# Performance work log

Hardware: AMD Instinct MI355X
Metric: run time of the kernel (lower is better)

The kernel has to match this reference:

```python
import jax, jax.numpy as jnp
import numpy as np

B, N, D_IN, D_OUT, H = 8, 1024, 768, 768, 12
D_HEAD = D_OUT // H  # 64; per-head softmax scale is sqrt(D_HEAD)


def setup_inputs() -> dict:
    key = jax.random.key(0)
    kx, kq, kk, kv, kwo, kbo = jax.random.split(key, 6)
    s_in = 1.0 / np.sqrt(D_IN)
    s_out = 1.0 / np.sqrt(D_OUT)
    return {
        "x": jax.random.normal(kx, (B, N, D_IN), dtype=jnp.float32),
        # stacked per-head Linear weights, torch layout [out, in] -> [H, d_head, D_IN]
        "Wq": jax.random.uniform(kq, (H, D_HEAD, D_IN), jnp.float32, -s_in, s_in),
        "Wk": jax.random.uniform(kk, (H, D_HEAD, D_IN), jnp.float32, -s_in, s_in),
        "Wv": jax.random.uniform(kv, (H, D_HEAD, D_IN), jnp.float32, -s_in, s_in),
        "Wo": jax.random.uniform(kwo, (D_OUT, D_OUT), jnp.float32, -s_out, s_out),
        "bo": jax.random.uniform(kbo, (D_OUT,), jnp.float32, -s_out, s_out),
    }


def reference(x, Wq, Wk, Wv, Wo, bo):
    # Per-head projections, batched over heads: [B, H, N, d_head]
    q = jnp.einsum('bnd,hed->bhne', x, Wq)
    k = jnp.einsum('bnd,hed->bhne', x, Wk)
    v = jnp.einsum('bnd,hed->bhne', x, Wv)
    scale = 1.0 / np.sqrt(D_HEAD)
    scores = jnp.einsum('bhie,bhje->bhij', q, k) * scale  # [B, H, N, N]
    att = jax.nn.softmax(scores, axis=-1)
    out = jnp.einsum('bhij,bhje->bhie', att, v)  # [B, H, N, d_head]
    # concat heads along last dim: [B, N, H*d_head]
    out = out.transpose(0, 2, 1, 3).reshape(B, N, D_OUT)
    return out @ Wo.T + bo
```

## Files before the change

### kernel.cpp

```cpp
#include <hip/hip_runtime.h>
#include <hip/hip_bf16.h>


typedef unsigned short u16;
typedef __attribute__((ext_vector_type(8))) short bf8;
typedef __attribute__((ext_vector_type(4))) short bf4;
typedef __attribute__((ext_vector_type(4))) float f4;
typedef __attribute__((ext_vector_type(4))) unsigned short us4;

#define NB 8
#define NSEQ 1024
#define DMODEL 768
#define NHEAD 12
#define DHEAD 64

#define XELEMS   (NB * NSEQ * DMODEL)
#define WELEMS   (DMODEL * DMODEL)

__device__ __forceinline__ float b2f(u16 u) {
  union { unsigned int i; float f; } c; c.i = ((unsigned int)u) << 16; return c.f;
}
__device__ __forceinline__ u16 f2b(float f) {
  union { float f; unsigned int i; } c; c.f = f;
  unsigned int r = c.i + 0x7fffu + ((c.i >> 16) & 1u);
  return (u16)(r >> 16);
}
__device__ __forceinline__ void gl_lds16(const u16* g, u16* l) {
  __builtin_amdgcn_global_load_lds(
      (const __attribute__((address_space(1))) unsigned int*)g,
      (__attribute__((address_space(3))) unsigned int*)l, 16, 0, 0);
}

struct CvtArgs {
  const float* src[5];
  u16* dst[5];
};
#define G0 (XELEMS / 4)
#define GW (WELEMS / 4)
#define GTOT (G0 + 4 * GW)

__global__ __launch_bounds__(256) void cvt_kernel(CvtArgs a) {
  size_t g = (size_t)blockIdx.x * 256 + threadIdx.x;
  if (g >= GTOT) return;
  int t; size_t off;
  if (g < G0) { t = 0; off = g; }
  else { size_t r = g - G0; t = 1 + (int)(r / GW); off = r % GW; }
  f4 v = *(const f4*)(a.src[t] + off * 4);
  us4 o;
  o[0] = f2b(v[0]); o[1] = f2b(v[1]); o[2] = f2b(v[2]); o[3] = f2b(v[3]);
  *(us4*)(a.dst[t] + off * 4) = o;
}

__global__ __launch_bounds__(256, 4) void qkv_gemm(
    const u16* __restrict__ x, const u16* __restrict__ Wq,
    const u16* __restrict__ Wk, const u16* __restrict__ Wv,
    u16* __restrict__ q, u16* __restrict__ k, u16* __restrict__ vt)
{
  __shared__ __align__(16) u16 lA[128 * 64];
  __shared__ __align__(16) u16 lB[128 * 64];

  const int tid  = threadIdx.x;
  const int lane = tid & 63;
  const int w    = tid >> 6;
  const int wm   = w >> 1, wn = w & 1;
  const int col  = lane & 15;
  const int quad = lane >> 4;
  const int bm = blockIdx.x;
  const int bn = blockIdx.y;

  const int m0 = bm * 128;
  const int proj = bn / 6;
  const u16* Wsel = (proj == 0) ? Wq : (proj == 1 ? Wk : Wv);
  const int nrem0 = (bn % 6) * 128;

  const int krow = lane >> 3;
  const int gsrc = (lane & 7) ^ krow;
  const u16* gA0 = x    + (size_t)(m0    + w * 32 + krow) * DMODEL + gsrc * 8;
  const u16* gB0 = Wsel + (size_t)(nrem0 + w * 32 + krow) * DMODEL + gsrc * 8;

  f4 acc[4][4];
#pragma unroll
  for (int i = 0; i < 4; i++)
#pragma unroll
    for (int j = 0; j < 4; j++) acc[i][j] = (f4)0.0f;

  for (int kk = 0; kk < DMODEL; kk += 64) {
    __syncthreads();
#pragma unroll
    for (int i = 0; i < 4; i++) {
      gl_lds16(gA0 + (size_t)(i * 8) * DMODEL + kk, lA + (w * 32 + i * 8) * 64);
      gl_lds16(gB0 + (size_t)(i * 8) * DMODEL + kk, lB + (w * 32 + i * 8) * 64);
    }
    __syncthreads();

#pragma unroll
    for (int kt = 0; kt < 2; kt++) {
      bf8 af[4], bfr[4];
#pragma unroll
      for (int mt = 0; mt < 4; mt++) {
        const int row = wm * 64 + mt * 16 + col;
        af[mt] = *(const bf8*)&lA[row * 64 + (((kt * 4 + quad) ^ (row & 7)) << 3)];
      }
#pragma unroll
      for (int nt = 0; nt < 4; nt++) {
        const int row = wn * 64 + nt * 16 + col;
        bfr[nt] = *(const bf8*)&lB[row * 64 + (((kt * 4 + quad) ^ (row & 7)) << 3)];
      }
#pragma unroll
      for (int mt = 0; mt < 4; mt++)
#pragma unroll
        for (int nt = 0; nt < 4; nt++)
          acc[mt][nt] = __builtin_amdgcn_mfma_f32_16x16x32_bf16(af[mt], bfr[nt], acc[mt][nt], 0, 0, 0);
    }
  }

  const int mw0 = m0 + wm * 64, nw0 = nrem0 + wn * 64;
  if (proj == 2) {
#pragma unroll
    for (int mt = 0; mt < 4; mt++) {
#pragma unroll
      for (int nt = 0; nt < 4; nt++) {
        const int nc = nw0 + nt * 16 + col;
        const int h = nc >> 6, e = nc & 63;
        const int t0 = mw0 + mt * 16 + quad * 4;
        const int b = t0 >> 10, tok0 = t0 & 1023;
        us4 pk;
#pragma unroll
        for (int r = 0; r < 4; r++) pk[r] = f2b(acc[mt][nt][r]);
        *(us4*)(vt + ((size_t)(b * NHEAD + h) * DHEAD + e) * NSEQ + tok0) = pk;
      }
    }
  } else {
    u16* dst = (proj == 0) ? q : k;
#pragma unroll
    for (int mt = 0; mt < 4; mt++) {
#pragma unroll
      for (int nt = 0; nt < 4; nt++) {
        const int nc = nw0 + nt * 16 + col;
        const int h = nc >> 6, e = nc & 63;
#pragma unroll
        for (int r = 0; r < 4; r++) {
          const int t = mw0 + mt * 16 + quad * 4 + r;
          const int b = t >> 10, tok = t & 1023;
          dst[((size_t)(b * NHEAD + h) * NSEQ + tok) * DHEAD + e] = f2b(acc[mt][nt][r]);
        }
      }
    }
  }
}

__global__ __launch_bounds__(256, 4) void attn_kernel(
    const u16* __restrict__ q, const u16* __restrict__ k,
    const u16* __restrict__ vt, u16* __restrict__ attn)
{
  __shared__ __align__(16) u16 ldsK[64 * 64];
  __shared__ __align__(16) u16 ldsV[64 * 64];
  __shared__ __align__(16) u16 ldsP[4][16][72];

  const int tid  = threadIdx.x;
  const int lane = tid & 63;
  const int w    = tid >> 6;
  const int col  = lane & 15;
  const int quad = lane >> 4;

  const int idx = blockIdx.x;
  const int bh = idx % 96, qc = idx / 96;
  const int b = bh / 12, h = bh % 12;

  const size_t head = ((size_t)b * NHEAD + h) * NSEQ * DHEAD;
  const int q0 = qc * 128 + w * 32;

  const int srow8 = lane >> 3;
  const int sg    = (lane & 7) ^ srow8;

  bf8 onesf;
#pragma unroll
  for (int j = 0; j < 8; j++) onesf[j] = (short)0x3F80;

  bf8 qf[2][2];
#pragma unroll
  for (int mt = 0; mt < 2; mt++)
#pragma unroll
    for (int kt = 0; kt < 2; kt++) {
      const int row = q0 + mt * 16 + col;
      bf8 t = *(const bf8*)(q + head + (size_t)row * DHEAD + kt * 32 + quad * 8);
#pragma unroll
      for (int j = 0; j < 8; j++) t[j] = (short)f2b(b2f((u16)t[j]) * 0.125f);
      qf[mt][kt] = t;
    }

  f4 lacc[2];
  f4 o[2][4];
#pragma unroll
  for (int mt = 0; mt < 2; mt++) {
    lacc[mt] = (f4)0.0f;
#pragma unroll
    for (int et = 0; et < 4; et++) o[mt][et] = (f4)0.0f;
  }

  for (int t = 0; t < NSEQ / 64; t++) {
    const int kbase = t * 64;

    __syncthreads();
#pragma unroll
    for (int i = 0; i < 2; i++) {
      const int li = w * 2 + i;
      gl_lds16(k  + head + (size_t)(kbase + li * 8 + srow8) * DHEAD + sg * 8,
               &ldsK[li * 512]);
      gl_lds16(vt + head + (size_t)(li * 8 + srow8) * NSEQ + kbase + sg * 8,
               &ldsV[li * 512]);
    }
    __syncthreads();

    f4 s[2][4];
#pragma unroll
    for (int mt = 0; mt < 2; mt++)
#pragma unroll
      for (int nt = 0; nt < 4; nt++) s[mt][nt] = (f4)0.0f;
#pragma unroll
    for (int kt = 0; kt < 2; kt++) {
      bf8 kf[4];
#pragma unroll
      for (int nt = 0; nt < 4; nt++) {
        const int row = nt * 16 + col;
        kf[nt] = *(const bf8*)&ldsK[row * 64 + (((kt * 4 + quad) ^ (col & 7)) << 3)];
      }
#pragma unroll
      for (int mt = 0; mt < 2; mt++)
#pragma unroll
        for (int nt = 0; nt < 4; nt++)
          s[mt][nt] = __builtin_amdgcn_mfma_f32_16x16x32_bf16(qf[mt][kt], kf[nt], s[mt][nt], 0, 0, 0);
    }

#pragma unroll
    for (int mt = 0; mt < 2; mt++) {
#pragma unroll
      for (int nt = 0; nt < 4; nt++)
#pragma unroll
        for (int r = 0; r < 4; r++)
          ldsP[w][quad * 4 + r][nt * 16 + col] = f2b(__expf(s[mt][nt][r]));
#pragma unroll
      for (int kt2 = 0; kt2 < 2; kt2++) {
        bf8 pf, vf[4];
        {
          const u16* pp = &ldsP[w][col][kt2 * 32 + quad * 8];
          bf4 lo = *(const bf4*)pp;
          bf4 hi = *(const bf4*)(pp + 4);
          pf = bf8{lo[0], lo[1], lo[2], lo[3], hi[0], hi[1], hi[2], hi[3]};
        }
        lacc[mt] = __builtin_amdgcn_mfma_f32_16x16x32_bf16(pf, onesf, lacc[mt], 0, 0, 0);
#pragma unroll
        for (int et = 0; et < 4; et++) {
          const int row = et * 16 + col;
          vf[et] = *(const bf8*)&ldsV[row * 64 + (((kt2 * 4 + quad) ^ (col & 7)) << 3)];
        }
#pragma unroll
        for (int et = 0; et < 4; et++)
          o[mt][et] = __builtin_amdgcn_mfma_f32_16x16x32_bf16(pf, vf[et], o[mt][et], 0, 0, 0);
      }
    }
  }

#pragma unroll
  for (int mt = 0; mt < 2; mt++)
#pragma unroll
    for (int r = 0; r < 4; r++) {
      const float inv = 1.0f / lacc[mt][r];
      const int token = q0 + mt * 16 + quad * 4 + r;
#pragma unroll
      for (int et = 0; et < 4; et++)
        attn[(size_t)(b * NSEQ + token) * DMODEL + h * DHEAD + et * 16 + col] =
            f2b(o[mt][et][r] * inv);
    }
}

__global__ __launch_bounds__(256, 4) void out_gemm(
    const u16* __restrict__ attn, const u16* __restrict__ Wo,
    const float* __restrict__ bo, float* __restrict__ out)
{
  __shared__ __align__(16) u16 lA[128 * 64];
  __shared__ __align__(16) u16 lB[128 * 64];

  const int tid  = threadIdx.x;
  const int lane = tid & 63;
  const int w    = tid >> 6;
  const int wm   = w >> 1, wn = w & 1;
  const int col  = lane & 15;
  const int quad = lane >> 4;
  const int bm = blockIdx.x;
  const int bn = blockIdx.y;

  const int m0 = bm * 128;
  const int n0 = bn * 128;

  const int krow = lane >> 3;
  const int gsrc = (lane & 7) ^ krow;
  const u16* gA0 = attn + (size_t)(m0 + w * 32 + krow) * DMODEL + gsrc * 8;
  const u16* gB0 = Wo   + (size_t)(n0 + w * 32 + krow) * DMODEL + gsrc * 8;

  f4 acc[4][4];
#pragma unroll
  for (int i = 0; i < 4; i++)
#pragma unroll
    for (int j = 0; j < 4; j++) acc[i][j] = (f4)0.0f;

  for (int kk = 0; kk < DMODEL; kk += 64) {
    __syncthreads();
#pragma unroll
    for (int i = 0; i < 4; i++) {
      gl_lds16(gA0 + (size_t)(i * 8) * DMODEL + kk, lA + (w * 32 + i * 8) * 64);
      gl_lds16(gB0 + (size_t)(i * 8) * DMODEL + kk, lB + (w * 32 + i * 8) * 64);
    }
    __syncthreads();

#pragma unroll
    for (int kt = 0; kt < 2; kt++) {
      bf8 af[4], bfr[4];
#pragma unroll
      for (int mt = 0; mt < 4; mt++) {
        const int row = wm * 64 + mt * 16 + col;
        af[mt] = *(const bf8*)&lA[row * 64 + (((kt * 4 + quad) ^ (row & 7)) << 3)];
      }
#pragma unroll
      for (int nt = 0; nt < 4; nt++) {
        const int row = wn * 64 + nt * 16 + col;
        bfr[nt] = *(const bf8*)&lB[row * 64 + (((kt * 4 + quad) ^ (row & 7)) << 3)];
      }
#pragma unroll
      for (int mt = 0; mt < 4; mt++)
#pragma unroll
        for (int nt = 0; nt < 4; nt++)
          acc[mt][nt] = __builtin_amdgcn_mfma_f32_16x16x32_bf16(af[mt], bfr[nt], acc[mt][nt], 0, 0, 0);
    }
  }

  const int mw0 = m0 + wm * 64, nw0 = n0 + wn * 64;
#pragma unroll
  for (int mt = 0; mt < 4; mt++)
#pragma unroll
    for (int nt = 0; nt < 4; nt++) {
      const int n = nw0 + nt * 16 + col;
      const float bias = bo[n];
#pragma unroll
      for (int r = 0; r < 4; r++) {
        const int row = mw0 + mt * 16 + quad * 4 + r;
        out[(size_t)row * DMODEL + n] = acc[mt][nt][r] + bias;
      }
    }
}

extern "C" void kernel_launch(void* const* d_in, const int* in_sizes, int n_in,
                              void* d_out, int out_size, void* d_ws, size_t ws_size,
                              hipStream_t stream) {
  const float* x  = (const float*)d_in[0];
  const float* Wq = (const float*)d_in[1];
  const float* Wk = (const float*)d_in[2];
  const float* Wv = (const float*)d_in[3];
  const float* Wo = (const float*)d_in[4];
  const float* bo = (const float*)d_in[5];
  float* out = (float*)d_out;

  u16* xb   = (u16*)d_ws;
  u16* wqb  = xb  + XELEMS;
  u16* wkb  = wqb + WELEMS;
  u16* wvb  = wkb + WELEMS;
  u16* wob  = wvb + WELEMS;
  u16* q    = wob + WELEMS;
  u16* k    = q   + XELEMS;
  u16* vt   = k   + XELEMS;
  u16* attn = vt  + XELEMS;

  CvtArgs ca;
  ca.src[0] = x;  ca.src[1] = Wq;  ca.src[2] = Wk;  ca.src[3] = Wv;  ca.src[4] = Wo;
  ca.dst[0] = xb; ca.dst[1] = wqb; ca.dst[2] = wkb; ca.dst[3] = wvb; ca.dst[4] = wob;

  cvt_kernel<<<dim3((GTOT + 255) / 256), 256, 0, stream>>>(ca);
  qkv_gemm<<<dim3(64, 18), 256, 0, stream>>>(xb, wqb, wkb, wvb, q, k, vt);
  attn_kernel<<<dim3(768), 256, 0, stream>>>(q, k, vt, attn);
  out_gemm<<<dim3(64, 6), 256, 0, stream>>>(attn, wob, bo, out);
}
```

Measured before the change: 197.9 us.

## Double-buffer LDS tiles in QKV, attention and output kernels with prefetch

The QKV and output GEMMs now keep two LDS buffers with a K-step of 32 instead of 64, and use a new XOR swizzle for the narrower rows. They issue the global-to-LDS load for the next K slice before computing on the current one, which leaves one barrier per iteration instead of two. The attention kernel likewise double-buffers its K and V tiles to prefetch the next key block during compute. Its occupancy hint drops from 4 to 3 blocks to make room for the larger shared-memory footprint. This is meant to hide global load latency behind MFMA work, at the cost of more LDS use, twice as many GEMM iterations and barriers, and lower attention occupancy.

```diff
diff --git a/kernel.cpp b/kernel.cpp
--- a/kernel.cpp
+++ b/kernel.cpp
@@ -56,8 +56,8 @@
     const u16* __restrict__ Wk, const u16* __restrict__ Wv,
     u16* __restrict__ q, u16* __restrict__ k, u16* __restrict__ vt)
 {
-  __shared__ __align__(16) u16 lA[128 * 64];
-  __shared__ __align__(16) u16 lB[128 * 64];
+  __shared__ __align__(16) u16 lA[2][128 * 32];
+  __shared__ __align__(16) u16 lB[2][128 * 32];
 
   const int tid  = threadIdx.x;
   const int lane = tid & 63;
@@ -73,10 +73,10 @@
   const u16* Wsel = (proj == 0) ? Wq : (proj == 1 ? Wk : Wv);
   const int nrem0 = (bn % 6) * 128;
 
-  const int krow = lane >> 3;
-  const int gsrc = (lane & 7) ^ krow;
-  const u16* gA0 = x    + (size_t)(m0    + w * 32 + krow) * DMODEL + gsrc * 8;
-  const u16* gB0 = Wsel + (size_t)(nrem0 + w * 32 + krow) * DMODEL + gsrc * 8;
+  const int srow = lane >> 2;
+  const int sg   = (lane & 3) ^ ((srow >> 1) & 3);
+  const u16* gA0 = x    + (size_t)(m0    + w * 32 + srow) * DMODEL + sg * 8;
+  const u16* gB0 = Wsel + (size_t)(nrem0 + w * 32 + srow) * DMODEL + sg * 8;
 
   f4 acc[4][4];
 #pragma unroll
@@ -84,34 +84,38 @@
 #pragma unroll
     for (int j = 0; j < 4; j++) acc[i][j] = (f4)0.0f;
 
-  for (int kk = 0; kk < DMODEL; kk += 64) {
+  gl_lds16(gA0, &lA[0][(w * 32) * 32]);
+  gl_lds16(gA0 + (size_t)16 * DMODEL, &lA[0][(w * 32 + 16) * 32]);
+  gl_lds16(gB0, &lB[0][(w * 32) * 32]);
+  gl_lds16(gB0 + (size_t)16 * DMODEL, &lB[0][(w * 32 + 16) * 32]);
+
+  for (int it = 0; it < 24; it++) {
+    const int cur = it & 1;
     __syncthreads();
-#pragma unroll
-    for (int i = 0; i < 4; i++) {
-      gl_lds16(gA0 + (size_t)(i * 8) * DMODEL + kk, lA + (w * 32 + i * 8) * 64);
-      gl_lds16(gB0 + (size_t)(i * 8) * DMODEL + kk, lB + (w * 32 + i * 8) * 64);
-    }
-    __syncthreads();
-
-#pragma unroll
-    for (int kt = 0; kt < 2; kt++) {
-      bf8 af[4], bfr[4];
-#pragma unroll
-      for (int mt = 0; mt < 4; mt++) {
-        const int row = wm * 64 + mt * 16 + col;
-        af[mt] = *(const bf8*)&lA[row * 64 + (((kt * 4 + quad) ^ (row & 7)) << 3)];
-      }
-#pragma unroll
-      for (int nt = 0; nt < 4; nt++) {
-        const int row = wn * 64 + nt * 16 + col;
-        bfr[nt] = *(const bf8*)&lB[row * 64 + (((kt * 4 + quad) ^ (row & 7)) << 3)];
-      }
-#pragma unroll
-      for (int mt = 0; mt < 4; mt++)
-#pragma unroll
-        for (int nt = 0; nt < 4; nt++)
-          acc[mt][nt] = __builtin_amdgcn_mfma_f32_16x16x32_bf16(af[mt], bfr[nt], acc[mt][nt], 0, 0, 0);
-    }
+    if (it < 23) {
+      const int kk = (it + 1) * 32;
+      gl_lds16(gA0 + kk, &lA[cur ^ 1][(w * 32) * 32]);
+      gl_lds16(gA0 + (size_t)16 * DMODEL + kk, &lA[cur ^ 1][(w * 32 + 16) * 32]);
+      gl_lds16(gB0 + kk, &lB[cur ^ 1][(w * 32) * 32]);
+      gl_lds16(gB0 + (size_t)16 * DMODEL + kk, &lB[cur ^ 1][(w * 32 + 16) * 32]);
+    }
+
+    bf8 af[4], bfr[4];
+#pragma unroll
+    for (int mt = 0; mt < 4; mt++) {
+      const int row = wm * 64 + mt * 16 + col;
+      af[mt] = *(const bf8*)&lA[cur][row * 32 + ((quad ^ ((row >> 1) & 3)) << 3)];
+    }
+#pragma unroll
+    for (int nt = 0; nt < 4; nt++) {
+      const int row = wn * 64 + nt * 16 + col;
+      bfr[nt] = *(const bf8*)&lB[cur][row * 32 + ((quad ^ ((row >> 1) & 3)) << 3)];
+    }
+#pragma unroll
+    for (int mt = 0; mt < 4; mt++)
+#pragma unroll
+      for (int nt = 0; nt < 4; nt++)
+        acc[mt][nt] = __builtin_amdgcn_mfma_f32_16x16x32_bf16(af[mt], bfr[nt], acc[mt][nt], 0, 0, 0);
   }
 
   const int mw0 = m0 + wm * 64, nw0 = nrem0 + wn * 64;
@@ -149,12 +153,12 @@
   }
 }
 
-__global__ __launch_bounds__(256, 4) void attn_kernel(
+__global__ __launch_bounds__(256, 3) void attn_kernel(
     const u16* __restrict__ q, const u16* __restrict__ k,
     const u16* __restrict__ vt, u16* __restrict__ attn)
 {
-  __shared__ __align__(16) u16 ldsK[64 * 64];
-  __shared__ __align__(16) u16 ldsV[64 * 64];
+  __shared__ __align__(16) u16 ldsK[2][64 * 64];
+  __shared__ __align__(16) u16 ldsV[2][64 * 64];
   __shared__ __align__(16) u16 ldsP[4][16][72];
 
   const int tid  = threadIdx.x;
@@ -198,19 +202,27 @@
     for (int et = 0; et < 4; et++) o[mt][et] = (f4)0.0f;
   }
 
+#pragma unroll
+  for (int i = 0; i < 2; i++) {
+    const int li = w * 2 + i;
+    gl_lds16(k  + head + (size_t)(li * 8 + srow8) * DHEAD + sg * 8, &ldsK[0][li * 512]);
+    gl_lds16(vt + head + (size_t)(li * 8 + srow8) * NSEQ + sg * 8,  &ldsV[0][li * 512]);
+  }
+
   for (int t = 0; t < NSEQ / 64; t++) {
-    const int kbase = t * 64;
-
+    const int cur = t & 1;
     __syncthreads();
-#pragma unroll
-    for (int i = 0; i < 2; i++) {
-      const int li = w * 2 + i;
-      gl_lds16(k  + head + (size_t)(kbase + li * 8 + srow8) * DHEAD + sg * 8,
-               &ldsK[li * 512]);
-      gl_lds16(vt + head + (size_t)(li * 8 + srow8) * NSEQ + kbase + sg * 8,
-               &ldsV[li * 512]);
-    }
-    __syncthreads();
+    if (t < NSEQ / 64 - 1) {
+      const int kb2 = (t + 1) * 64;
+#pragma unroll
+      for (int i = 0; i < 2; i++) {
+        const int li = w * 2 + i;
+        gl_lds16(k  + head + (size_t)(kb2 + li * 8 + srow8) * DHEAD + sg * 8,
+                 &ldsK[cur ^ 1][li * 512]);
+        gl_lds16(vt + head + (size_t)(li * 8 + srow8) * NSEQ + kb2 + sg * 8,
+                 &ldsV[cur ^ 1][li * 512]);
+      }
+    }
 
     f4 s[2][4];
 #pragma unroll
@@ -223,7 +235,7 @@
 #pragma unroll
       for (int nt = 0; nt < 4; nt++) {
         const int row = nt * 16 + col;
-        kf[nt] = *(const bf8*)&ldsK[row * 64 + (((kt * 4 + quad) ^ (col & 7)) << 3)];
+        kf[nt] = *(const bf8*)&ldsK[cur][row * 64 + (((kt * 4 + quad) ^ (col & 7)) << 3)];
       }
 #pragma unroll
       for (int mt = 0; mt < 2; mt++)
@@ -252,7 +264,7 @@
 #pragma unroll
         for (int et = 0; et < 4; et++) {
           const int row = et * 16 + col;
-          vf[et] = *(const bf8*)&ldsV[row * 64 + (((kt2 * 4 + quad) ^ (col & 7)) << 3)];
+          vf[et] = *(const bf8*)&ldsV[cur][row * 64 + (((kt2 * 4 + quad) ^ (col & 7)) << 3)];
         }
 #pragma unroll
         for (int et = 0; et < 4; et++)
@@ -278,8 +290,8 @@
     const u16* __restrict__ attn, const u16* __restrict__ Wo,
     const float* __restrict__ bo, float* __restrict__ out)
 {
-  __shared__ __align__(16) u16 lA[128 * 64];
-  __shared__ __align__(16) u16 lB[128 * 64];
+  __shared__ __align__(16) u16 lA[2][128 * 32];
+  __shared__ __align__(16) u16 lB[2][128 * 32];
 
   const int tid  = threadIdx.x;
   const int lane = tid & 63;
@@ -293,10 +305,10 @@
   const int m0 = bm * 128;
   const int n0 = bn * 128;
 
-  const int krow = lane >> 3;
-  const int gsrc = (lane & 7) ^ krow;
-  const u16* gA0 = attn + (size_t)(m0 + w * 32 + krow) * DMODEL + gsrc * 8;
-  const u16* gB0 = Wo   + (size_t)(n0 + w * 32 + krow) * DMODEL + gsrc * 8;
+  const int srow = lane >> 2;
+  const int sg   = (lane & 3) ^ ((srow >> 1) & 3);
+  const u16* gA0 = attn + (size_t)(m0 + w * 32 + srow) * DMODEL + sg * 8;
+  const u16* gB0 = Wo   + (size_t)(n0 + w * 32 + srow) * DMODEL + sg * 8;
 
   f4 acc[4][4];
 #pragma unroll
@@ -304,34 +316,38 @@
 #pragma unroll
     for (int j = 0; j < 4; j++) acc[i][j] = (f4)0.0f;
 
-  for (int kk = 0; kk < DMODEL; kk += 64) {
+  gl_lds16(gA0, &lA[0][(w * 32) * 32]);
+  gl_lds16(gA0 + (size_t)16 * DMODEL, &lA[0][(w * 32 + 16) * 32]);
+  gl_lds16(gB0, &lB[0][(w * 32) * 32]);
+  gl_lds16(gB0 + (size_t)16 * DMODEL, &lB[0][(w * 32 + 16) * 32]);
+
+  for (int it = 0; it < 24; it++) {
+    const int cur = it & 1;
     __syncthreads();
-#pragma unroll
-    for (int i = 0; i < 4; i++) {
-      gl_lds16(gA0 + (size_t)(i * 8) * DMODEL + kk, lA + (w * 32 + i * 8) * 64);
-      gl_lds16(gB0 + (size_t)(i * 8) * DMODEL + kk, lB + (w * 32 + i * 8) * 64);
-    }
-    __syncthreads();
-
-#pragma unroll
-    for (int kt = 0; kt < 2; kt++) {
-      bf8 af[4], bfr[4];
-#pragma unroll
-      for (int mt = 0; mt < 4; mt++) {
-        const int row = wm * 64 + mt * 16 + col;
-        af[mt] = *(const bf8*)&lA[row * 64 + (((kt * 4 + quad) ^ (row & 7)) << 3)];
-      }
-#pragma unroll
-      for (int nt = 0; nt < 4; nt++) {
-        const int row = wn * 64 + nt * 16 + col;
-        bfr[nt] = *(const bf8*)&lB[row * 64 + (((kt * 4 + quad) ^ (row & 7)) << 3)];
-      }
-#pragma unroll
-      for (int mt = 0; mt < 4; mt++)
-#pragma unroll
-        for (int nt = 0; nt < 4; nt++)
-          acc[mt][nt] = __builtin_amdgcn_mfma_f32_16x16x32_bf16(af[mt], bfr[nt], acc[mt][nt], 0, 0, 0);
-    }
+    if (it < 23) {
+      const int kk = (it + 1) * 32;
+      gl_lds16(gA0 + kk, &lA[cur ^ 1][(w * 32) * 32]);
+      gl_lds16(gA0 + (size_t)16 * DMODEL + kk, &lA[cur ^ 1][(w * 32 + 16) * 32]);
+      gl_lds16(gB0 + kk, &lB[cur ^ 1][(w * 32) * 32]);
+      gl_lds16(gB0 + (size_t)16 * DMODEL + kk, &lB[cur ^ 1][(w * 32 + 16) * 32]);
+    }
+
+    bf8 af[4], bfr[4];
+#pragma unroll
+    for (int mt = 0; mt < 4; mt++) {
+      const int row = wm * 64 + mt * 16 + col;
+      af[mt] = *(const bf8*)&lA[cur][row * 32 + ((quad ^ ((row >> 1) & 3)) << 3)];
+    }
+#pragma unroll
+    for (int nt = 0; nt < 4; nt++) {
+      const int row = wn * 64 + nt * 16 + col;
+      bfr[nt] = *(const bf8*)&lB[cur][row * 32 + ((quad ^ ((row >> 1) & 3)) << 3)];
+    }
+#pragma unroll
+    for (int mt = 0; mt < 4; mt++)
+#pragma unroll
+      for (int nt = 0; nt < 4; nt++)
+        acc[mt][nt] = __builtin_amdgcn_mfma_f32_16x16x32_bf16(af[mt], bfr[nt], acc[mt][nt], 0, 0, 0);
   }
 
   const int mw0 = m0 + wm * 64, nw0 = n0 + wn * 64;
```

Result: no change. 196.1 us (-0.9%).
